# Kernel tuning notes

Hardware: AMD Instinct MI355X
Metric: run time of the kernel (lower is better)

Reference implementation:

```python
import jax, jax.numpy as jnp
import numpy as np

T, H, NH, NKV, HD = 2048, 1024, 16, 4, 64
I, E, TOPK = 2048, 8, 2
EPS = 1e-5
ROPE_BASE = 10000.0


def rms_norm(x, w):
    var = jnp.mean(x * x, axis=-1, keepdims=True)
    return x * jax.lax.rsqrt(var + EPS) * w


def apply_rope(x, positions, n_heads):
    # neox-style rotary over full head_dim
    t = x.reshape(-1, n_heads, HD)
    half = HD // 2
    inv_freq = 1.0 / (ROPE_BASE ** (jnp.arange(0, half, dtype=jnp.float32) / half))
    freqs = positions.astype(jnp.float32)[:, None] * inv_freq[None, :]  # [T, half]
    cos = jnp.cos(freqs)[:, None, :]
    sin = jnp.sin(freqs)[:, None, :]
    x1, x2 = t[..., :half], t[..., half:]
    rot = jnp.concatenate([x1 * cos - x2 * sin, x2 * cos + x1 * sin], axis=-1)
    return rot.reshape(x.shape)


def setup_inputs():
    key = jax.random.key(0)
    ks = jax.random.split(key, 9)
    s = 0.02
    return dict(
        positions=jnp.arange(T, dtype=jnp.int32),
        hidden_states=jax.random.normal(ks[0], (T, H), jnp.float32),
        input_ln_w=jnp.ones((H,), jnp.float32),
        post_ln_w=jnp.ones((H,), jnp.float32),
        residual_ln_w=jnp.ones((H,), jnp.float32),
        qkv_w=jax.random.normal(ks[1], ((NH + 2 * NKV) * HD, H), jnp.float32) * s,
        o_w=jax.random.normal(ks[2], (H, NH * HD), jnp.float32) * s,
        gate_w=jax.random.normal(ks[3], (E, H), jnp.float32) * s,
        ws=jax.random.normal(ks[4], (E, 2 * I, H), jnp.float32) * s,
        w2s=jax.random.normal(ks[5], (E, H, I), jnp.float32) * s,
        res_w13=jax.random.normal(ks[6], (2 * H, H), jnp.float32) * s,
        res_w2=jax.random.normal(ks[7], (H, H), jnp.float32) * s,
    )


def attention(x, positions, qkv_w, o_w):
    qkv = x @ qkv_w.T  # [T, (NH+2*NKV)*HD]
    q, k, v = jnp.split(qkv, [NH * HD, NH * HD + NKV * HD], axis=-1)
    q = apply_rope(q, positions, NH)
    k = apply_rope(k, positions, NKV)
    q = q.reshape(T, NH, HD)
    k = k.reshape(T, NKV, HD)
    v = v.reshape(T, NKV, HD)
    rep = NH // NKV  # GQA: repeat kv heads
    k = jnp.repeat(k, rep, axis=1)
    v = jnp.repeat(v, rep, axis=1)
    scale = HD ** -0.5
    scores = jnp.einsum('tnd,snd->nts', q, k) * scale  # [NH, T, T]
    causal = jnp.tril(jnp.ones((T, T), dtype=bool))
    scores = jnp.where(causal[None], scores, -jnp.inf)
    probs = jax.nn.softmax(scores, axis=-1)
    out = jnp.einsum('nts,snd->tnd', probs, v).reshape(T, NH * HD)
    return out @ o_w.T


def silu_and_mul(gu):
    g, u = jnp.split(gu, 2, axis=-1)
    return jax.nn.silu(g) * u


def moe(x, gate_w, ws, w2s):
    logits = x @ gate_w.T  # [T, E]
    probs = jax.nn.softmax(logits, axis=-1)
    topk_w, topk_ids = jax.lax.top_k(probs, TOPK)
    topk_w = topk_w / jnp.sum(topk_w, axis=-1, keepdims=True)  # renormalize (top_k > 1)
    routes = jnp.zeros((x.shape[0], E), x.dtype).at[
        jnp.arange(x.shape[0])[:, None], topk_ids].set(topk_w)  # [T, E] sparse routing
    gu = jnp.einsum('th,eih->tei', x, ws)        # [T, E, 2I]
    act = silu_and_mul(gu)                        # [T, E, I]
    eo = jnp.einsum('tei,ehi->teh', act, w2s)     # [T, E, H]
    return jnp.einsum('te,teh->th', routes, eo)


def reference(positions, hidden_states, input_ln_w, post_ln_w, residual_ln_w,
              qkv_w, o_w, gate_w, ws, w2s, res_w13, res_w2):
    residual_input = hidden_states
    h = rms_norm(hidden_states, input_ln_w)
    h = attention(h, positions, qkv_w, o_w)
    residual_attn = residual_input + h
    # parallel residual MLP branch (ffn_dim == hidden)
    r = rms_norm(residual_attn, residual_ln_w)
    r = silu_and_mul(r @ res_w13.T) @ res_w2.T
    residual_mlp = residual_attn + r
    # MoE branch
    m = rms_norm(residual_attn, post_ln_w)
    m = moe(m, gate_w, ws, w2s)
    return residual_mlp + m
```

## Files before the change

kernel.cpp:

```cpp
#include <hip/hip_runtime.h>
#include <stdint.h>


typedef _Float16 f16;
typedef _Float16 f16x8 __attribute__((ext_vector_type(8)));
typedef _Float16 f16x4 __attribute__((ext_vector_type(4)));
typedef float f32x4 __attribute__((ext_vector_type(4)));

#define DEV __device__ __forceinline__

DEV void glds16(const void* g, void* l) {
  __builtin_amdgcn_global_load_lds((const __attribute__((address_space(1))) void*)g,
                                   (__attribute__((address_space(3))) void*)l, 16, 0, 0);
}

__global__ void cvt_f16_kernel(const float* __restrict__ in, f16* __restrict__ outp) {
  const size_t i = ((size_t)blockIdx.x * 256 + threadIdx.x) * 4;
  float4 f = *(const float4*)(in + i);
  f16x4 o;
  o[0] = (f16)f.x; o[1] = (f16)f.y; o[2] = (f16)f.z; o[3] = (f16)f.w;
  *(f16x4*)(outp + i) = o;
}

__global__ void cvt_f16x2_kernel(const float* __restrict__ in,
                                 f16* __restrict__ oh, f16* __restrict__ ol) {
  const size_t i = ((size_t)blockIdx.x * 256 + threadIdx.x) * 4;
  float4 f = *(const float4*)(in + i);
  f16x4 h, l;
  h[0] = (f16)f.x; l[0] = (f16)(f.x - (float)h[0]);
  h[1] = (f16)f.y; l[1] = (f16)(f.y - (float)h[1]);
  h[2] = (f16)f.z; l[2] = (f16)(f.z - (float)h[2]);
  h[3] = (f16)f.w; l[3] = (f16)(f.w - (float)h[3]);
  *(f16x4*)(oh + i) = h;
  *(f16x4*)(ol + i) = l;
}

__global__ void rmsnorm_kernel(const float* __restrict__ in, const float* __restrict__ w,
                               f16* __restrict__ outp) {
  const int t = blockIdx.x * 4 + (threadIdx.x >> 6);
  const int lane = threadIdx.x & 63;
  const float* x = in + (size_t)t * 1024;
  float v[16]; float ss = 0.f;
#pragma unroll
  for (int j = 0; j < 16; j++) { float a = x[lane + 64 * j]; v[j] = a; ss += a * a; }
#pragma unroll
  for (int m = 1; m < 64; m <<= 1) ss += __shfl_xor(ss, m);
  const float rs = rsqrtf(ss * (1.f / 1024.f) + 1e-5f);
#pragma unroll
  for (int j = 0; j < 16; j++)
    outp[(size_t)t * 1024 + lane + 64 * j] = (f16)(v[j] * rs * w[lane + 64 * j]);
}

__global__ void rmsnorm_dual_kernel(const float* __restrict__ in,
                                    const float* __restrict__ w1, const float* __restrict__ w2,
                                    f16* __restrict__ o1, f16* __restrict__ o2) {
  const int t = blockIdx.x * 4 + (threadIdx.x >> 6);
  const int lane = threadIdx.x & 63;
  const float* x = in + (size_t)t * 1024;
  float v[16]; float ss = 0.f;
#pragma unroll
  for (int j = 0; j < 16; j++) { float a = x[lane + 64 * j]; v[j] = a; ss += a * a; }
#pragma unroll
  for (int m = 1; m < 64; m <<= 1) ss += __shfl_xor(ss, m);
  const float rs = rsqrtf(ss * (1.f / 1024.f) + 1e-5f);
#pragma unroll
  for (int j = 0; j < 16; j++) {
    float nv = v[j] * rs;
    size_t idx = (size_t)t * 1024 + lane + 64 * j;
    o1[idx] = (f16)(nv * w1[lane + 64 * j]);
    o2[idx] = (f16)(nv * w2[lane + 64 * j]);
  }
}

template <int EPI, int BN, int SPLITK = 1>
__global__ __launch_bounds__(256) void gemm_f16_kernel(
    const f16* __restrict__ A, const f16* __restrict__ B,
    void* __restrict__ outp, const float* __restrict__ addsrc,
    int M, int N, int K) {
  constexpr int JT = BN / 32;
  constexpr int L = (BN == 128) ? 4 : 3;
  __shared__ __attribute__((aligned(16))) f16 As[3][128 * 32];
  __shared__ __attribute__((aligned(16))) f16 Bs[3][BN * 32];
  const int tid = threadIdx.x;
  const size_t row0 = (size_t)blockIdx.y * 128, col0 = (size_t)blockIdx.x * BN;
  const int ks = (SPLITK > 1) ? (int)blockIdx.z : 0;
  const int kspan = K / SPLITK, kb = ks * kspan;
  const int nt = kspan >> 5;
  const int c0 = tid, c1 = tid + 256;
  const int sw0 = ((c0 & 3) ^ ((c0 >> 3) & 3)) * 8;
  const int sw1 = ((c1 & 3) ^ ((c1 >> 3) & 3)) * 8;
  const f16* a0 = A + (row0 + (c0 >> 2)) * K + sw0;
  const f16* a1 = A + (row0 + (c1 >> 2)) * K + sw1;
  const f16* b0 = B + (col0 + (c0 >> 2)) * K + sw0;
  const f16* b1 = B + (col0 + ((BN == 128) ? (c1 >> 2) : 0)) * K + ((BN == 128) ? sw1 : 0);

  const int wave = tid >> 6, lane = tid & 63, lr = lane >> 4, lc = lane & 15;
  const int wr = wave >> 1, wc = wave & 1;
  const int rsw = (lr ^ ((lc >> 1) & 3)) * 8;

  f32x4 acc[4][JT];
#pragma unroll
  for (int i = 0; i < 4; i++)
#pragma unroll
    for (int j = 0; j < JT; j++) acc[i][j] = (f32x4){0.f, 0.f, 0.f, 0.f};

  auto stage = [&](int k0, int buf) {
    glds16(a0 + k0, As[buf] + c0 * 8);
    glds16(a1 + k0, As[buf] + c1 * 8);
    glds16(b0 + k0, Bs[buf] + c0 * 8);
    if constexpr (BN == 128) glds16(b1 + k0, Bs[buf] + c1 * 8);
  };

  stage(kb, 0); stage(kb + 32, 1);
  for (int t = 0; t < nt; ++t) {
    if (t < nt - 1) asm volatile("s_waitcnt vmcnt(%0)" :: "n"(L) : "memory");
    else            asm volatile("s_waitcnt vmcnt(0)" ::: "memory");
    __builtin_amdgcn_s_barrier();
    asm volatile("" ::: "memory");
    if (t + 2 < nt) stage(kb + (t + 2) * 32, (t + 2) % 3);
    const f16* Ab = As[t % 3];
    const f16* Bb = Bs[t % 3];
    f16x8 af[4], bfr[JT];
#pragma unroll
    for (int i = 0; i < 4; i++)
      af[i] = *(const f16x8*)(Ab + (wr * 64 + i * 16 + lc) * 32 + rsw);
#pragma unroll
    for (int j = 0; j < JT; j++)
      bfr[j] = *(const f16x8*)(Bb + (wc * (BN / 2) + j * 16 + lc) * 32 + rsw);
#pragma unroll
    for (int i = 0; i < 4; i++)
#pragma unroll
      for (int j = 0; j < JT; j++)
        acc[i][j] = __builtin_amdgcn_mfma_f32_16x16x32_f16(af[i], bfr[j], acc[i][j], 0, 0, 0);
  }

#pragma unroll
  for (int i = 0; i < 4; i++)
#pragma unroll
    for (int j = 0; j < JT; j++) {
      const size_t rbase = row0 + wr * 64 + i * 16 + lr * 4;
      const size_t col = col0 + wc * (BN / 2) + j * 16 + lc;
#pragma unroll
      for (int r = 0; r < 4; r++) {
        size_t idx = (rbase + r) * N + col;
        if constexpr (SPLITK > 1) {
          ((float*)outp)[(size_t)ks * M * N + idx] = acc[i][j][r];
        } else if constexpr (EPI == 0) ((float*)outp)[idx] = acc[i][j][r];
        else if constexpr (EPI == 1) ((float*)outp)[idx] = acc[i][j][r] + addsrc[idx];
        else ((f16*)outp)[idx] = (f16)acc[i][j][r];
      }
    }
}

template <int SPLITK>
__global__ __launch_bounds__(256) void gemm_f16x2_add_kernel(
    const f16* __restrict__ Ah, const f16* __restrict__ Al,
    const f16* __restrict__ Bh, const f16* __restrict__ Bl,
    float* __restrict__ outp, const float* __restrict__ addsrc,
    int M, int N, int K) {
  __shared__ __attribute__((aligned(16))) f16 Ash[3][128 * 32];
  __shared__ __attribute__((aligned(16))) f16 Asl[3][128 * 32];
  __shared__ __attribute__((aligned(16))) f16 Bsh[3][64 * 32];
  __shared__ __attribute__((aligned(16))) f16 Bsl[3][64 * 32];
  const int tid = threadIdx.x;
  const size_t row0 = (size_t)blockIdx.y * 128, col0 = (size_t)blockIdx.x * 64;
  const int ks = (SPLITK > 1) ? (int)blockIdx.z : 0;
  const int kspan = K / SPLITK, kb = ks * kspan;
  const int nt = kspan >> 5;
  const int c0 = tid, c1 = tid + 256;
  const int sw0 = ((c0 & 3) ^ ((c0 >> 3) & 3)) * 8;
  const int sw1 = ((c1 & 3) ^ ((c1 >> 3) & 3)) * 8;
  const size_t aoff0 = (row0 + (c0 >> 2)) * K + sw0;
  const size_t aoff1 = (row0 + (c1 >> 2)) * K + sw1;
  const size_t boff0 = (col0 + (c0 >> 2)) * K + sw0;

  const int wave = tid >> 6, lane = tid & 63, lr = lane >> 4, lc = lane & 15;
  const int wr = wave >> 1, wc = wave & 1;
  const int rsw = (lr ^ ((lc >> 1) & 3)) * 8;

  f32x4 acc[4][2];
#pragma unroll
  for (int i = 0; i < 4; i++)
#pragma unroll
    for (int j = 0; j < 2; j++) acc[i][j] = (f32x4){0.f, 0.f, 0.f, 0.f};

  auto stage = [&](int k0, int buf) {
    glds16(Ah + aoff0 + k0, Ash[buf] + c0 * 8);
    glds16(Ah + aoff1 + k0, Ash[buf] + c1 * 8);
    glds16(Al + aoff0 + k0, Asl[buf] + c0 * 8);
    glds16(Al + aoff1 + k0, Asl[buf] + c1 * 8);
    glds16(Bh + boff0 + k0, Bsh[buf] + c0 * 8);
    glds16(Bl + boff0 + k0, Bsl[buf] + c0 * 8);
  };

  stage(kb, 0); stage(kb + 32, 1);
  for (int t = 0; t < nt; ++t) {
    if (t < nt - 1) asm volatile("s_waitcnt vmcnt(%0)" :: "n"(6) : "memory");
    else            asm volatile("s_waitcnt vmcnt(0)" ::: "memory");
    __builtin_amdgcn_s_barrier();
    asm volatile("" ::: "memory");
    if (t + 2 < nt) stage(kb + (t + 2) * 32, (t + 2) % 3);
    const int bc = t % 3;
    f16x8 afh[4], afl[4], bfh[2], bfl[2];
#pragma unroll
    for (int i = 0; i < 4; i++) {
      const int ro = (wr * 64 + i * 16 + lc) * 32 + rsw;
      afh[i] = *(const f16x8*)(Ash[bc] + ro);
      afl[i] = *(const f16x8*)(Asl[bc] + ro);
    }
#pragma unroll
    for (int j = 0; j < 2; j++) {
      const int ro = (wc * 32 + j * 16 + lc) * 32 + rsw;
      bfh[j] = *(const f16x8*)(Bsh[bc] + ro);
      bfl[j] = *(const f16x8*)(Bsl[bc] + ro);
    }
#pragma unroll
    for (int i = 0; i < 4; i++)
#pragma unroll
      for (int j = 0; j < 2; j++) {
        acc[i][j] = __builtin_amdgcn_mfma_f32_16x16x32_f16(afh[i], bfh[j], acc[i][j], 0, 0, 0);
        acc[i][j] = __builtin_amdgcn_mfma_f32_16x16x32_f16(afh[i], bfl[j], acc[i][j], 0, 0, 0);
        acc[i][j] = __builtin_amdgcn_mfma_f32_16x16x32_f16(afl[i], bfh[j], acc[i][j], 0, 0, 0);
      }
  }

#pragma unroll
  for (int i = 0; i < 4; i++)
#pragma unroll
    for (int j = 0; j < 2; j++) {
      const size_t rbase = row0 + wr * 64 + i * 16 + lr * 4;
      const size_t col = col0 + wc * 32 + j * 16 + lc;
#pragma unroll
      for (int r = 0; r < 4; r++) {
        size_t idx = (rbase + r) * N + col;
        if constexpr (SPLITK > 1) outp[(size_t)ks * M * N + idx] = acc[i][j][r];
        else outp[idx] = acc[i][j][r] + addsrc[idx];
      }
    }
}

template <int DIVROW, int BN, int SPLITK = 1>
__global__ __launch_bounds__(256) void gemm_moe_kernel(
    const f16* __restrict__ A, const f16* __restrict__ Ball, void* __restrict__ outp,
    const int* __restrict__ perm, const int* __restrict__ counts,
    int N, int K, size_t strideB) {
  constexpr int JT = BN / 32;
  constexpr int L = (BN == 128) ? 4 : 3;
  const int e = (int)blockIdx.z / SPLITK;
  const int ks = (int)blockIdx.z % SPLITK;
  const int cnt = counts[e];
  const int bm = blockIdx.y;
  if (bm * 128 >= cnt) return;
  const int kspan = K / SPLITK, kb = ks * kspan;
  const int nt = kspan >> 5;
  const f16* B = Ball + (size_t)e * strideB;
  __shared__ __attribute__((aligned(16))) f16 As[3][128 * 32];
  __shared__ __attribute__((aligned(16))) f16 Bs[3][BN * 32];
  const int tid = threadIdx.x;
  const size_t col0 = (size_t)blockIdx.x * BN;
  const int c0 = tid, c1 = tid + 256;
  const int pbase = e * 2048 + bm * 128;
  const int rt0 = c0 >> 2, rt1 = c1 >> 2;
  const int sid0 = (bm * 128 + rt0 < cnt) ? perm[pbase + rt0] : 0;
  const int sid1 = (bm * 128 + rt1 < cnt) ? perm[pbase + rt1] : 0;
  const size_t ar0 = DIVROW ? (size_t)(sid0 >> 1) : (size_t)sid0;
  const size_t ar1 = DIVROW ? (size_t)(sid1 >> 1) : (size_t)sid1;
  const int sw0 = ((c0 & 3) ^ ((c0 >> 3) & 3)) * 8;
  const int sw1 = ((c1 & 3) ^ ((c1 >> 3) & 3)) * 8;
  const f16* ap0 = A + ar0 * K + sw0;
  const f16* ap1 = A + ar1 * K + sw1;
  const f16* b0 = B + (col0 + (c0 >> 2)) * K + sw0;
  const f16* b1 = B + (col0 + ((BN == 128) ? (c1 >> 2) : 0)) * K + ((BN == 128) ? sw1 : 0);

  const int wave = tid >> 6, lane = tid & 63, lr = lane >> 4, lc = lane & 15;
  const int wr = wave >> 1, wc = wave & 1;
  const int rsw = (lr ^ ((lc >> 1) & 3)) * 8;

  f32x4 acc[4][JT];
#pragma unroll
  for (int i = 0; i < 4; i++)
#pragma unroll
    for (int j = 0; j < JT; j++) acc[i][j] = (f32x4){0.f, 0.f, 0.f, 0.f};

  auto stage = [&](int k0, int buf) {
    glds16(ap0 + k0, As[buf] + c0 * 8);
    glds16(ap1 + k0, As[buf] + c1 * 8);
    glds16(b0 + k0, Bs[buf] + c0 * 8);
    if constexpr (BN == 128) glds16(b1 + k0, Bs[buf] + c1 * 8);
  };

  stage(kb, 0); stage(kb + 32, 1);
  for (int t = 0; t < nt; ++t) {
    if (t < nt - 1) asm volatile("s_waitcnt vmcnt(%0)" :: "n"(L) : "memory");
    else            asm volatile("s_waitcnt vmcnt(0)" ::: "memory");
    __builtin_amdgcn_s_barrier();
    asm volatile("" ::: "memory");
    if (t + 2 < nt) stage(kb + (t + 2) * 32, (t + 2) % 3);
    const f16* Ab = As[t % 3];
    const f16* Bb = Bs[t % 3];
    f16x8 af[4], bfr[JT];
#pragma unroll
    for (int i = 0; i < 4; i++)
      af[i] = *(const f16x8*)(Ab + (wr * 64 + i * 16 + lc) * 32 + rsw);
#pragma unroll
    for (int j = 0; j < JT; j++)
      bfr[j] = *(const f16x8*)(Bb + (wc * (BN / 2) + j * 16 + lc) * 32 + rsw);
#pragma unroll
    for (int i = 0; i < 4; i++)
#pragma unroll
      for (int j = 0; j < JT; j++)
        acc[i][j] = __builtin_amdgcn_mfma_f32_16x16x32_f16(af[i], bfr[j], acc[i][j], 0, 0, 0);
  }

  int sids[4][4];
#pragma unroll
  for (int i = 0; i < 4; i++)
#pragma unroll
    for (int r = 0; r < 4; r++) {
      int rit = wr * 64 + i * 16 + lr * 4 + r;
      sids[i][r] = (bm * 128 + rit < cnt) ? perm[pbase + rit] : -1;
    }
#pragma unroll
  for (int i = 0; i < 4; i++)
#pragma unroll
    for (int j = 0; j < JT; j++) {
      const size_t col = col0 + wc * (BN / 2) + j * 16 + lc;
#pragma unroll
      for (int r = 0; r < 4; r++)
        if (sids[i][r] >= 0) {
          if constexpr (SPLITK > 1)
            ((float*)outp)[((size_t)ks * 4096 + sids[i][r]) * N + col] = acc[i][j][r];
          else
            ((f16*)outp)[(size_t)sids[i][r] * N + col] = (f16)acc[i][j][r];
        }
    }
}

__global__ void rope_table_kernel(const int* __restrict__ pos, float2* __restrict__ tab) {
  const int idx = blockIdx.x * 256 + threadIdx.x;
  const int t = idx >> 5, i = idx & 31;
  const double ph = (double)pos[t] * exp((double)i * -0.28782313662425575);
  tab[idx] = make_float2((float)cos(ph), (float)sin(ph));
}

__global__ void rope_kernel(const float* __restrict__ qkv, const float2* __restrict__ tab,
                            f16* __restrict__ qr, f16* __restrict__ kr) {
  const int t = blockIdx.y;
  const int u = blockIdx.x * 256 + threadIdx.x;
  if (u >= 640) return;
  const float* b0 = qkv + (size_t)t * 1536;
  const float* b1 = b0 + (size_t)2048 * 1536;
  const int head = u >> 5, i = u & 31;
  const bool isq = head < 16;
  const int off = isq ? head * 64 + i : 1024 + (head - 16) * 64 + i;
  const float x1 = b0[off] + b1[off], x2 = b0[off + 32] + b1[off + 32];
  const float2 cs = tab[t * 32 + i];
  const float c = cs.x, s = cs.y;
  const float r1 = x1 * c - x2 * s, r2 = x2 * c + x1 * s;
  if (isq) {
    const float qs = 0.18033688011116042f;
    qr[(size_t)t * 1024 + head * 64 + i] = (f16)(qs * r1);
    qr[(size_t)t * 1024 + head * 64 + i + 32] = (f16)(qs * r2);
  } else {
    const int kh = head - 16;
    kr[(size_t)t * 256 + kh * 64 + i] = (f16)r1;
    kr[(size_t)t * 256 + kh * 64 + i + 32] = (f16)r2;
  }
}

__global__ void vtrans_kernel(const float* __restrict__ qkvf, f16* __restrict__ vt) {
  __shared__ float Ts[64 * 69];
  const int t0 = blockIdx.x * 64;
  const int kv = blockIdx.y;
  const int tid = threadIdx.x;
  const int tr = tid >> 2, jj = tid & 3;
  const float* src0 = qkvf + (size_t)(t0 + tr) * 1536 + 1280 + kv * 64 + jj * 16;
  const float* src1 = src0 + (size_t)2048 * 1536;
#pragma unroll
  for (int x = 0; x < 4; x++) {
    float4 f = *(const float4*)(src0 + x * 4);
    float4 g = *(const float4*)(src1 + x * 4);
    Ts[tr * 69 + jj * 16 + x * 4 + 0] = f.x + g.x;
    Ts[tr * 69 + jj * 16 + x * 4 + 1] = f.y + g.y;
    Ts[tr * 69 + jj * 16 + x * 4 + 2] = f.z + g.z;
    Ts[tr * 69 + jj * 16 + x * 4 + 3] = f.w + g.w;
  }
  __syncthreads();
  f16* dst = vt + (size_t)(kv * 64 + tr) * 2048 + t0 + jj * 16;
#pragma unroll
  for (int x = 0; x < 2; x++) {
    f16x8 o;
#pragma unroll
    for (int i = 0; i < 8; i++) o[i] = (f16)Ts[(jj * 16 + x * 8 + i) * 69 + tr];
    *(f16x8*)(dst + x * 8) = o;
  }
}

__global__ void add3_kernel(float* __restrict__ o, const float* __restrict__ a,
                            const float* __restrict__ p0, const float* __restrict__ p1) {
  const size_t i4 = ((size_t)blockIdx.x * 256 + threadIdx.x) * 4;
  float4 va = *(const float4*)(a + i4);
  float4 v0 = *(const float4*)(p0 + i4);
  float4 v1 = *(const float4*)(p1 + i4);
  va.x += v0.x + v1.x;
  va.y += v0.y + v1.y;
  va.z += v0.z + v1.z;
  va.w += v0.w + v1.w;
  *(float4*)(o + i4) = va;
}

__global__ __launch_bounds__(256, 3) void attn_kernel(
    const f16* __restrict__ qr, const f16* __restrict__ kr, const f16* __restrict__ vt,
    f16* __restrict__ ahi, f16* __restrict__ alo) {
  const int qt = 31 - (int)blockIdx.x;
  const int h = blockIdx.y;
  const int kvh = h >> 2;
  __shared__ __attribute__((aligned(16))) f16 Ks[128 * 72];
  __shared__ __attribute__((aligned(16))) f16 Vs[64 * 136];
  __shared__ __attribute__((aligned(16))) f16 Pl[4 * 16 * 136];
  const int tid = threadIdx.x;
  const int wave = tid >> 6, lane = tid & 63, lr = lane >> 4, lc = lane & 15;
  const int trow = qt * 64 + wave * 16 + lc;
  f16* Pw = Pl + wave * 16 * 136;

  const int krow = tid >> 3, kcol = (tid & 7) * 8;
  const int vrow = tid >> 4, vcol = (tid & 15) * 8;
  const f16* kgbase = kr + (size_t)kvh * 64 + kcol;
  const f16* vgbase = vt + (size_t)(kvh * 64 + vrow) * 2048 + vcol;

  const f16* qp = qr + (size_t)trow * 1024 + h * 64 + lr * 8;
  f16x8 qf0 = *(const f16x8*)(qp);
  f16x8 qf1 = *(const f16x8*)(qp + 32);

  float m_run = -3e38f, l_run = 0.f;
  f32x4 accO[4];
#pragma unroll
  for (int jo = 0; jo < 4; jo++) accO[jo] = (f32x4){0.f, 0.f, 0.f, 0.f};

  const int nch = (qt >> 1) + 1;

  f16x8 kreg[4], vreg[4];
#pragma unroll
  for (int it = 0; it < 4; it++) {
    kreg[it] = *(const f16x8*)(kgbase + (size_t)(it * 32 + krow) * 256);
    vreg[it] = *(const f16x8*)(vgbase + it * 16 * 2048);
  }

  for (int ch = 0; ch < nch; ++ch) {
    const int c0 = ch * 128;
    const bool last = (ch == nch - 1);

    __syncthreads();
#pragma unroll
    for (int it = 0; it < 4; it++) {
      *(f16x8*)(Ks + (it * 32 + krow) * 72 + kcol) = kreg[it];
      *(f16x8*)(Vs + (it * 16 + vrow) * 136 + vcol) = vreg[it];
    }
    __syncthreads();

    if (!last) {
      const int c1 = c0 + 128;
#pragma unroll
      for (int it = 0; it < 4; it++) {
        kreg[it] = *(const f16x8*)(kgbase + (size_t)(c1 + it * 32 + krow) * 256);
        vreg[it] = *(const f16x8*)(vgbase + it * 16 * 2048 + c1);
      }
    }

    f32x4 st[8];
#pragma unroll
    for (int j = 0; j < 8; j++) {
      const f16* kp = Ks + (j * 16 + lc) * 72 + lr * 8;
      f16x8 ka0 = *(const f16x8*)(kp);
      f16x8 ka1 = *(const f16x8*)(kp + 32);
      f32x4 s = (f32x4){0.f, 0.f, 0.f, 0.f};
      s = __builtin_amdgcn_mfma_f32_16x16x32_f16(ka0, qf0, s, 0, 0, 0);
      s = __builtin_amdgcn_mfma_f32_16x16x32_f16(ka1, qf1, s, 0, 0, 0);
      st[j] = s;
    }

    if (last) {
#pragma unroll
      for (int j = 0; j < 8; j++)
#pragma unroll
        for (int r = 0; r < 4; r++)
          if (c0 + j * 16 + lr * 4 + r > trow) st[j][r] = -3e38f;
    }

    float mc = -3e38f;
#pragma unroll
    for (int j = 0; j < 8; j++)
      mc = fmaxf(mc, fmaxf(fmaxf(st[j][0], st[j][1]), fmaxf(st[j][2], st[j][3])));
    mc = fmaxf(mc, __shfl_xor(mc, 16));
    mc = fmaxf(mc, __shfl_xor(mc, 32));
    const float mn = fmaxf(m_run, mc);
    const float alpha = __builtin_amdgcn_exp2f(m_run - mn);
    m_run = mn;

    float ls = 0.f;
#pragma unroll
    for (int j = 0; j < 8; j++) {
      f16x4 pv;
#pragma unroll
      for (int r = 0; r < 4; r++) {
        float e = __builtin_amdgcn_exp2f(st[j][r] - mn);
        ls += e;
        pv[r] = (f16)e;
      }
      *(f16x4*)(Pw + lc * 136 + j * 16 + lr * 4) = pv;
    }
    ls += __shfl_xor(ls, 16);
    ls += __shfl_xor(ls, 32);
    l_run = l_run * alpha + ls;
#pragma unroll
    for (int jo = 0; jo < 4; jo++) accO[jo] *= alpha;

#pragma unroll
    for (int kkt = 0; kkt < 4; kkt++) {
      f16x8 pb = *(const f16x8*)(Pw + lc * 136 + kkt * 32 + lr * 8);
#pragma unroll
      for (int jo = 0; jo < 4; jo++) {
        f16x8 va = *(const f16x8*)(Vs + (jo * 16 + lc) * 136 + kkt * 32 + lr * 8);
        accO[jo] = __builtin_amdgcn_mfma_f32_16x16x32_f16(va, pb, accO[jo], 0, 0, 0);
      }
    }
  }

  const float inv = 1.f / l_run;
#pragma unroll
  for (int jo = 0; jo < 4; jo++) {
    f16x4 hi4, lo4;
#pragma unroll
    for (int r = 0; r < 4; r++) {
      float o = accO[jo][r] * inv;
      f16 hv = (f16)o;
      hi4[r] = hv;
      lo4[r] = (f16)(o - (float)hv);
    }
    const size_t idx = (size_t)trow * 1024 + h * 64 + jo * 16 + lr * 4;
    *(f16x4*)(ahi + idx) = hi4;
    *(f16x4*)(alo + idx) = lo4;
  }
}

__global__ void routing_kernel(const float* __restrict__ resA,
                               const float* __restrict__ postw,
                               const float* __restrict__ gw,
                               int* __restrict__ counts, int* __restrict__ perm,
                               float* __restrict__ rw) {
  const int t = blockIdx.x * 4 + (threadIdx.x >> 6);
  const int lane = threadIdx.x & 63;
  const float* x = resA + (size_t)t * 1024;
  float v[16]; float ss = 0.f;
#pragma unroll
  for (int j = 0; j < 16; j++) { float a = x[lane + 64 * j]; v[j] = a; ss += a * a; }
#pragma unroll
  for (int m = 1; m < 64; m <<= 1) ss += __shfl_xor(ss, m);
  const float rs = rsqrtf(ss * (1.f / 1024.f) + 1e-5f);
#pragma unroll
  for (int j = 0; j < 16; j++) v[j] *= rs * postw[lane + 64 * j];
  float lg[8];
#pragma unroll
  for (int e = 0; e < 8; e++) {
    float p = 0.f;
    const float* g = gw + (size_t)e * 1024;
#pragma unroll
    for (int j = 0; j < 16; j++) p += v[j] * g[lane + 64 * j];
#pragma unroll
    for (int m = 1; m < 64; m <<= 1) p += __shfl_xor(p, m);
    lg[e] = p;
  }
  if (lane == 0) {
    int e0 = 0; float b0 = lg[0];
#pragma unroll
    for (int e = 1; e < 8; e++) if (lg[e] > b0) { b0 = lg[e]; e0 = e; }
    int e1 = -1; float b1 = -3e38f;
#pragma unroll
    for (int e = 0; e < 8; e++) if (e != e0 && lg[e] > b1) { b1 = lg[e]; e1 = e; }
    const float w0 = 1.f / (1.f + expf(b1 - b0));
    const float w1 = 1.f - w0;
    int p0 = atomicAdd(&counts[e0], 1);
    perm[e0 * 2048 + p0] = t * 2;
    int p1 = atomicAdd(&counts[e1], 1);
    perm[e1 * 2048 + p1] = t * 2 + 1;
    rw[t * 2] = w0;
    rw[t * 2 + 1] = w1;
  }
}

__global__ void silu_mul_kernel(const f16* __restrict__ gu, f16* __restrict__ outp, int lgN) {
  const int N = 1 << lgN;
  const size_t i4 = ((size_t)blockIdx.x * 256 + threadIdx.x) * 4;
  const size_t r = i4 >> lgN;
  const int c = (int)(i4 & (N - 1));
  const f16* gp = gu + r * (size_t)(2 * N) + c;
  f16x4 g = *(const f16x4*)gp;
  f16x4 u = *(const f16x4*)(gp + N);
  f16x4 o;
#pragma unroll
  for (int x = 0; x < 4; x++) {
    float gg = (float)g[x], uu = (float)u[x];
    o[x] = (f16)(gg / (1.f + __expf(-gg)) * uu);
  }
  *(f16x4*)(outp + r * (size_t)N + c) = o;
}

__global__ void final_add2_kernel(float* __restrict__ outp, const float* __restrict__ eo2,
                                  const float* __restrict__ rw) {
  const size_t i4 = ((size_t)blockIdx.x * 256 + threadIdx.x) * 4;
  const int t = (int)(i4 >> 10);
  const int c = (int)(i4 & 1023);
  const float w0 = rw[2 * t], w1 = rw[2 * t + 1];
  float4 s0 = {0.f, 0.f, 0.f, 0.f}, s1 = {0.f, 0.f, 0.f, 0.f};
#pragma unroll
  for (int ks = 0; ks < 2; ks++) {
    const float* p = eo2 + (size_t)ks * 4096 * 1024;
    float4 a = *(const float4*)(p + (size_t)(2 * t) * 1024 + c);
    float4 b = *(const float4*)(p + (size_t)(2 * t + 1) * 1024 + c);
    s0.x += a.x; s0.y += a.y; s0.z += a.z; s0.w += a.w;
    s1.x += b.x; s1.y += b.y; s1.z += b.z; s1.w += b.w;
  }
  float4 o = *(float4*)(outp + i4);
  o.x += w0 * s0.x + w1 * s1.x;
  o.y += w0 * s0.y + w1 * s1.y;
  o.z += w0 * s0.z + w1 * s1.z;
  o.w += w0 * s0.w + w1 * s1.w;
  *(float4*)(outp + i4) = o;
}

extern "C" void kernel_launch(void* const* d_in, const int* in_sizes, int n_in,
                              void* d_out, int out_size, void* d_ws, size_t ws_size,
                              hipStream_t stream) {
  const int* positions = (const int*)d_in[0];
  const float* hidden = (const float*)d_in[1];
  const float* in_ln = (const float*)d_in[2];
  const float* post_ln = (const float*)d_in[3];
  const float* res_ln = (const float*)d_in[4];
  const float* qkv_w = (const float*)d_in[5];
  const float* o_w = (const float*)d_in[6];
  const float* gate_w = (const float*)d_in[7];
  const float* ws_w = (const float*)d_in[8];
  const float* w2s_w = (const float*)d_in[9];
  const float* w13_w = (const float*)d_in[10];
  const float* w2_w = (const float*)d_in[11];
  float* out = (float*)d_out;

  char* p = (char*)d_ws;
  auto alloc = [&](size_t b) { void* r = (void*)p; p += (b + 255) & ~(size_t)255; return r; };

  f16* wqkv = (f16*)alloc((size_t)1536 * 1024 * 2);
  f16* woh  = (f16*)alloc((size_t)1024 * 1024 * 2);
  f16* wol  = (f16*)alloc((size_t)1024 * 1024 * 2);
  f16* wws  = (f16*)alloc((size_t)8 * 4096 * 1024 * 2);
  f16* ww2  = (f16*)alloc((size_t)8 * 1024 * 2048 * 2);
  f16* w13  = (f16*)alloc((size_t)2048 * 1024 * 2);
  f16* w2c  = (f16*)alloc((size_t)1024 * 1024 * 2);
  f16* hn   = (f16*)alloc((size_t)2048 * 1024 * 2);
  float* qkvp = (float*)alloc((size_t)2 * 2048 * 1536 * 4);
  float2* ptab = (float2*)alloc((size_t)2048 * 32 * 8);
  f16* qr = (f16*)alloc((size_t)2048 * 1024 * 2);
  f16* kr = (f16*)alloc((size_t)2048 * 256 * 2);
  f16* vt = (f16*)alloc((size_t)256 * 2048 * 2);
  f16* ath = (f16*)alloc((size_t)2048 * 1024 * 2);
  f16* atl = (f16*)alloc((size_t)2048 * 1024 * 2);
  float* opp = (float*)alloc((size_t)2 * 2048 * 1024 * 4);
  float* resA = (float*)alloc((size_t)2048 * 1024 * 4);
  f16* rn = (f16*)alloc((size_t)2048 * 1024 * 2);
  f16* mn = (f16*)alloc((size_t)2048 * 1024 * 2);
  f16* gu13 = (f16*)alloc((size_t)2048 * 2048 * 2);
  f16* act13 = (f16*)alloc((size_t)2048 * 1024 * 2);
  float* w2p = (float*)alloc((size_t)2 * 2048 * 1024 * 4);
  f16* gum = (f16*)alloc((size_t)4096 * 4096 * 2);
  f16* actm = (f16*)alloc((size_t)4096 * 2048 * 2);
  float* eo2 = (float*)alloc((size_t)2 * 4096 * 1024 * 4);
  float* rw = (float*)alloc((size_t)4096 * 4);
  int* counts = (int*)alloc(256);
  int* perm = (int*)alloc((size_t)8 * 2048 * 4);

  cvt_f16_kernel<<<dim3(1536 * 1024 / 1024), dim3(256), 0, stream>>>(qkv_w, wqkv);
  cvt_f16_kernel<<<dim3(8 * 4096 * 1024 / 1024), dim3(256), 0, stream>>>(ws_w, wws);
  cvt_f16_kernel<<<dim3(8 * 1024 * 2048 / 1024), dim3(256), 0, stream>>>(w2s_w, ww2);
  cvt_f16_kernel<<<dim3(2048 * 1024 / 1024), dim3(256), 0, stream>>>(w13_w, w13);
  cvt_f16_kernel<<<dim3(1024 * 1024 / 1024), dim3(256), 0, stream>>>(w2_w, w2c);
  cvt_f16x2_kernel<<<dim3(1024 * 1024 / 1024), dim3(256), 0, stream>>>(o_w, woh, wol);
  rope_table_kernel<<<dim3(256), dim3(256), 0, stream>>>(positions, ptab);
  hipMemsetAsync(counts, 0, 256, stream);

  rmsnorm_kernel<<<dim3(512), dim3(256), 0, stream>>>(hidden, in_ln, hn);
  gemm_f16_kernel<0, 64, 2><<<dim3(24, 16, 2), dim3(256), 0, stream>>>(
      hn, wqkv, (void*)qkvp, (const float*)nullptr, 2048, 1536, 1024);
  rope_kernel<<<dim3(3, 2048), dim3(256), 0, stream>>>(qkvp, ptab, qr, kr);
  vtrans_kernel<<<dim3(32, 4), dim3(256), 0, stream>>>(qkvp, vt);
  attn_kernel<<<dim3(32, 16), dim3(256), 0, stream>>>(qr, kr, vt, ath, atl);
  gemm_f16x2_add_kernel<2><<<dim3(16, 16, 2), dim3(256), 0, stream>>>(
      ath, atl, woh, wol, opp, (const float*)nullptr, 2048, 1024, 1024);
  add3_kernel<<<dim3(2048), dim3(256), 0, stream>>>(
      resA, hidden, opp, opp + (size_t)2048 * 1024);

  rmsnorm_dual_kernel<<<dim3(512), dim3(256), 0, stream>>>(resA, res_ln, post_ln, rn, mn);
  routing_kernel<<<dim3(512), dim3(256), 0, stream>>>(resA, post_ln, gate_w, counts, perm, rw);

  gemm_f16_kernel<2, 64><<<dim3(32, 16), dim3(256), 0, stream>>>(
      rn, w13, (void*)gu13, (const float*)nullptr, 2048, 2048, 1024);
  silu_mul_kernel<<<dim3(2048 * 1024 / 1024), dim3(256), 0, stream>>>(gu13, act13, 10);
  gemm_f16_kernel<0, 64, 2><<<dim3(16, 16, 2), dim3(256), 0, stream>>>(
      act13, w2c, (void*)w2p, (const float*)nullptr, 2048, 1024, 1024);
  add3_kernel<<<dim3(2048), dim3(256), 0, stream>>>(
      out, resA, w2p, w2p + (size_t)2048 * 1024);

  gemm_moe_kernel<1, 128><<<dim3(32, 16, 8), dim3(256), 0, stream>>>(
      mn, wws, (void*)gum, perm, counts, 4096, 1024, (size_t)4096 * 1024);
  silu_mul_kernel<<<dim3(4096 * 2048 / 1024), dim3(256), 0, stream>>>(gum, actm, 11);
  gemm_moe_kernel<0, 128, 2><<<dim3(8, 16, 16), dim3(256), 0, stream>>>(
      actm, ww2, (void*)eo2, perm, counts, 1024, 2048, (size_t)1024 * 2048);
  final_add2_kernel<<<dim3(2048 * 1024 / 1024), dim3(256), 0, stream>>>(out, eo2, rw);
}
```

Measured before the change: 622.2 us.

## Fuse MoE gate/up GEMM with SiLU-mul epilogue and raise MFMA wave priority

Adds a MoE gate/up GEMM kernel that loads matching gate and up weight rows into separate LDS tiles, accumulates both products, and applies SiLU(g)*u in the epilogue, writing the activation directly. This removes the 4096x4096 f16 intermediate buffer, its write and re-read, and the separate silu_mul launch. It also wraps the MFMA loops in the MoE GEMM and attention kernels with s_setprio so math waves get scheduling priority. The fused kernel holds twice the accumulators per thread, which may raise register pressure and lower occupancy.

```diff
diff --git a/kernel.cpp b/kernel.cpp
--- a/kernel.cpp
+++ b/kernel.cpp
@@ -236,6 +236,108 @@
         if constexpr (SPLITK > 1) outp[(size_t)ks * M * N + idx] = acc[i][j][r];
         else outp[idx] = acc[i][j][r] + addsrc[idx];
       }
+    }
+}
+
+__global__ __launch_bounds__(256) void gemm_moe_gated_kernel(
+    const f16* __restrict__ A, const f16* __restrict__ Ball, f16* __restrict__ actm,
+    const int* __restrict__ perm, const int* __restrict__ counts,
+    int K, size_t strideB) {
+  const int e = (int)blockIdx.z;
+  const int cnt = counts[e];
+  const int bm = blockIdx.y;
+  if (bm * 128 >= cnt) return;
+  const int nt = K >> 5;
+  const f16* B = Ball + (size_t)e * strideB;
+  __shared__ __attribute__((aligned(16))) f16 As[3][128 * 32];
+  __shared__ __attribute__((aligned(16))) f16 Bgs[3][64 * 32];
+  __shared__ __attribute__((aligned(16))) f16 Bus[3][64 * 32];
+  const int tid = threadIdx.x;
+  const size_t col0 = (size_t)blockIdx.x * 64;
+  const int c0 = tid, c1 = tid + 256;
+  const int pbase = e * 2048 + bm * 128;
+  const int rt0 = c0 >> 2, rt1 = c1 >> 2;
+  const int sid0 = (bm * 128 + rt0 < cnt) ? perm[pbase + rt0] : 0;
+  const int sid1 = (bm * 128 + rt1 < cnt) ? perm[pbase + rt1] : 0;
+  const size_t ar0 = (size_t)(sid0 >> 1);
+  const size_t ar1 = (size_t)(sid1 >> 1);
+  const int sw0 = ((c0 & 3) ^ ((c0 >> 3) & 3)) * 8;
+  const int sw1 = ((c1 & 3) ^ ((c1 >> 3) & 3)) * 8;
+  const f16* ap0 = A + ar0 * K + sw0;
+  const f16* ap1 = A + ar1 * K + sw1;
+  const f16* bg0 = B + (col0 + (c0 >> 2)) * K + sw0;
+  const f16* bu0 = B + (2048 + col0 + (c0 >> 2)) * K + sw0;
+
+  const int wave = tid >> 6, lane = tid & 63, lr = lane >> 4, lc = lane & 15;
+  const int wr = wave >> 1, wc = wave & 1;
+  const int rsw = (lr ^ ((lc >> 1) & 3)) * 8;
+
+  f32x4 accg[4][2], accu[4][2];
+#pragma unroll
+  for (int i = 0; i < 4; i++)
+#pragma unroll
+    for (int j = 0; j < 2; j++) {
+      accg[i][j] = (f32x4){0.f, 0.f, 0.f, 0.f};
+      accu[i][j] = (f32x4){0.f, 0.f, 0.f, 0.f};
+    }
+
+  auto stage = [&](int k0, int buf) {
+    glds16(ap0 + k0, As[buf] + c0 * 8);
+    glds16(ap1 + k0, As[buf] + c1 * 8);
+    glds16(bg0 + k0, Bgs[buf] + c0 * 8);
+    glds16(bu0 + k0, Bus[buf] + c0 * 8);
+  };
+
+  stage(0, 0); stage(32, 1);
+  for (int t = 0; t < nt; ++t) {
+    if (t < nt - 1) asm volatile("s_waitcnt vmcnt(%0)" :: "n"(4) : "memory");
+    else            asm volatile("s_waitcnt vmcnt(0)" ::: "memory");
+    __builtin_amdgcn_s_barrier();
+    asm volatile("" ::: "memory");
+    if (t + 2 < nt) stage((t + 2) * 32, (t + 2) % 3);
+    const f16* Ab = As[t % 3];
+    const f16* Bgb = Bgs[t % 3];
+    const f16* Bub = Bus[t % 3];
+    f16x8 af[4], bg[2], bu[2];
+#pragma unroll
+    for (int i = 0; i < 4; i++)
+      af[i] = *(const f16x8*)(Ab + (wr * 64 + i * 16 + lc) * 32 + rsw);
+#pragma unroll
+    for (int j = 0; j < 2; j++) {
+      const int ro = (wc * 32 + j * 16 + lc) * 32 + rsw;
+      bg[j] = *(const f16x8*)(Bgb + ro);
+      bu[j] = *(const f16x8*)(Bub + ro);
+    }
+    __builtin_amdgcn_s_setprio(1);
+#pragma unroll
+    for (int i = 0; i < 4; i++)
+#pragma unroll
+      for (int j = 0; j < 2; j++) {
+        accg[i][j] = __builtin_amdgcn_mfma_f32_16x16x32_f16(af[i], bg[j], accg[i][j], 0, 0, 0);
+        accu[i][j] = __builtin_amdgcn_mfma_f32_16x16x32_f16(af[i], bu[j], accu[i][j], 0, 0, 0);
+      }
+    __builtin_amdgcn_s_setprio(0);
+  }
+
+  int sids[4][4];
+#pragma unroll
+  for (int i = 0; i < 4; i++)
+#pragma unroll
+    for (int r = 0; r < 4; r++) {
+      int rit = wr * 64 + i * 16 + lr * 4 + r;
+      sids[i][r] = (bm * 128 + rit < cnt) ? perm[pbase + rit] : -1;
+    }
+#pragma unroll
+  for (int i = 0; i < 4; i++)
+#pragma unroll
+    for (int j = 0; j < 2; j++) {
+      const size_t col = col0 + wc * 32 + j * 16 + lc;
+#pragma unroll
+      for (int r = 0; r < 4; r++)
+        if (sids[i][r] >= 0) {
+          const float g = accg[i][j][r], u = accu[i][j][r];
+          actm[(size_t)sids[i][r] * 2048 + col] = (f16)(g / (1.f + __expf(-g)) * u);
+        }
     }
 }
 
@@ -305,11 +407,13 @@
 #pragma unroll
     for (int j = 0; j < JT; j++)
       bfr[j] = *(const f16x8*)(Bb + (wc * (BN / 2) + j * 16 + lc) * 32 + rsw);
+    __builtin_amdgcn_s_setprio(1);
 #pragma unroll
     for (int i = 0; i < 4; i++)
 #pragma unroll
       for (int j = 0; j < JT; j++)
         acc[i][j] = __builtin_amdgcn_mfma_f32_16x16x32_f16(af[i], bfr[j], acc[i][j], 0, 0, 0);
+    __builtin_amdgcn_s_setprio(0);
   }
 
   int sids[4][4];
@@ -468,6 +572,7 @@
     }
 
     f32x4 st[8];
+    __builtin_amdgcn_s_setprio(1);
 #pragma unroll
     for (int j = 0; j < 8; j++) {
       const f16* kp = Ks + (j * 16 + lc) * 72 + lr * 8;
@@ -478,6 +583,7 @@
       s = __builtin_amdgcn_mfma_f32_16x16x32_f16(ka1, qf1, s, 0, 0, 0);
       st[j] = s;
     }
+    __builtin_amdgcn_s_setprio(0);
 
     if (last) {
 #pragma unroll
@@ -515,6 +621,7 @@
 #pragma unroll
     for (int jo = 0; jo < 4; jo++) accO[jo] *= alpha;
 
+    __builtin_amdgcn_s_setprio(1);
 #pragma unroll
     for (int kkt = 0; kkt < 4; kkt++) {
       f16x8 pb = *(const f16x8*)(Pw + lc * 136 + kkt * 32 + lr * 8);
@@ -524,6 +631,7 @@
         accO[jo] = __builtin_amdgcn_mfma_f32_16x16x32_f16(va, pb, accO[jo], 0, 0, 0);
       }
     }
+    __builtin_amdgcn_s_setprio(0);
   }
 
   const float inv = 1.f / l_run;
@@ -670,7 +778,6 @@
   f16* gu13 = (f16*)alloc((size_t)2048 * 2048 * 2);
   f16* act13 = (f16*)alloc((size_t)2048 * 1024 * 2);
   float* w2p = (float*)alloc((size_t)2 * 2048 * 1024 * 4);
-  f16* gum = (f16*)alloc((size_t)4096 * 4096 * 2);
   f16* actm = (f16*)alloc((size_t)4096 * 2048 * 2);
   float* eo2 = (float*)alloc((size_t)2 * 4096 * 1024 * 4);
   float* rw = (float*)alloc((size_t)4096 * 4);
@@ -708,9 +815,8 @@
   add3_kernel<<<dim3(2048), dim3(256), 0, stream>>>(
       out, resA, w2p, w2p + (size_t)2048 * 1024);
 
-  gemm_moe_kernel<1, 128><<<dim3(32, 16, 8), dim3(256), 0, stream>>>(
-      mn, wws, (void*)gum, perm, counts, 4096, 1024, (size_t)4096 * 1024);
-  silu_mul_kernel<<<dim3(4096 * 2048 / 1024), dim3(256), 0, stream>>>(gum, actm, 11);
+  gemm_moe_gated_kernel<<<dim3(32, 16, 8), dim3(256), 0, stream>>>(
+      mn, wws, actm, perm, counts, 1024, (size_t)4096 * 1024);
   gemm_moe_kernel<0, 128, 2><<<dim3(8, 16, 16), dim3(256), 0, stream>>>(
       actm, ww2, (void*)eo2, perm, counts, 1024, 2048, (size_t)1024 * 2048);
   final_add2_kernel<<<dim3(2048 * 1024 / 1024), dim3(256), 0, stream>>>(out, eo2, rw);
```

Measured after the change: 611.6 us. Within noise of the previous version (-1.7%).
